# Performance work log

Measured on AMD Instinct MI355X. Metric: run time of the kernel, lower is better.

## Reference

```python
import jax, jax.numpy as jnp
import numpy as np

N_NODES = 100000
N_EDGES = 3200000
IN_DIM = 128
HIDDEN = 128
N_GRAPHS = 64


def setup_inputs() -> dict:
    key = jax.random.key(0)
    ks = jax.random.split(key, 16)
    feat = jax.random.normal(ks[0], (N_NODES, IN_DIM), dtype=jnp.float32)
    src = jax.random.randint(ks[1], (N_EDGES,), 0, N_NODES, dtype=jnp.int32)
    dst = jax.random.randint(ks[2], (N_EDGES,), 0, N_NODES, dtype=jnp.int32)
    graph_ids = jnp.sort(jax.random.randint(ks[3], (N_NODES,), 0, N_GRAPHS, dtype=jnp.int32))
    # GraphConv weights (in_feats, out_feats) + bias, DGL default glorot-ish scale
    def lin(k, fi, fo):
        s = 1.0 / np.sqrt(fi)
        kw, kb = jax.random.split(k)
        W = jax.random.uniform(kw, (fi, fo), jnp.float32, -s, s)
        b = jax.random.uniform(kb, (fo,), jnp.float32, -s, s)
        return W, b
    W1, b1 = lin(ks[4], IN_DIM, HIDDEN)
    W2, b2 = lin(ks[5], HIDDEN, HIDDEN)
    # MLPReadout(128, 1, L=3): 128->64->32->16->1
    Wm0, bm0 = lin(ks[6], 128, 64)
    Wm1, bm1 = lin(ks[7], 64, 32)
    Wm2, bm2 = lin(ks[8], 32, 16)
    Wm3, bm3 = lin(ks[9], 16, 1)
    return dict(feat=feat, src=src, dst=dst, graph_ids=graph_ids, num_graphs=N_GRAPHS,
                W1=W1, b1=b1, W2=W2, b2=b2,
                Wm0=Wm0, bm0=bm0, Wm1=Wm1, bm1=bm1, Wm2=Wm2, bm2=bm2, Wm3=Wm3, bm3=bm3)


def reference(feat, src, dst, graph_ids, num_graphs,
              W1, b1, W2, b2,
              Wm0, bm0, Wm1, bm1, Wm2, bm2, Wm3, bm3):
    N = feat.shape[0]
    ones_e = jnp.ones(src.shape[0], dtype=feat.dtype)
    # DGL GraphConv norm='both': D_out^{-1/2} on src side, D_in^{-1/2} on dst side,
    # degrees clamped to >=1 (allow_zero_in_degree=True)
    deg_out = jnp.clip(jax.ops.segment_sum(ones_e, src, num_segments=N), 1.0)
    deg_in = jnp.clip(jax.ops.segment_sum(ones_e, dst, num_segments=N), 1.0)
    norm_src = jax.lax.rsqrt(deg_out)[:, None]  # [N,1]
    norm_dst = jax.lax.rsqrt(deg_in)[:, None]

    def gconv(h, W, b):
        h = h * norm_src
        agg = jax.ops.segment_sum(h[src], dst, num_segments=N)  # SpMM: [N,d]
        return agg * norm_dst @ W + b

    h = jax.nn.relu(gconv(feat, W1, b1))
    h = jax.nn.relu(gconv(h, W2, b2))

    # dgl.mean_nodes: per-graph mean over nodes
    counts = jnp.clip(jax.ops.segment_sum(jnp.ones(N, dtype=h.dtype), graph_ids, num_segments=num_graphs), 1.0)
    hg = jax.ops.segment_sum(h, graph_ids, num_segments=num_graphs) / counts[:, None]  # [G, hidden]

    # MLPReadout
    y = jax.nn.relu(hg @ Wm0 + bm0)
    y = jax.nn.relu(y @ Wm1 + bm1)
    y = jax.nn.relu(y @ Wm2 + bm2)
    return y @ Wm3 + bm3  # [G, 1]
```

## Files before the change

### kernel.cpp

```cpp
#include <hip/hip_runtime.h>
#include <hip/hip_fp16.h>

#define N_NODES 100000
#define N_EDGES 3200000
#define DIM 128
#define NG 64
#define GS_CHUNKS 16

#define KSH 8
#define BKT 256
#define NBKT ((N_NODES + BKT - 1) / BKT)
#define CHUNK 8192
#define NBLK ((N_EDGES + CHUNK - 1) / CHUNK)

using f16x8 = __attribute__((ext_vector_type(8))) _Float16;
using f32x4 = __attribute__((ext_vector_type(4))) float;

__global__ __launch_bounds__(256) void k_hist1(const int* __restrict__ src, const int* __restrict__ dst,
                                               int* __restrict__ histD, int* __restrict__ histS,
                                               int* __restrict__ rowtot) {
    __shared__ int hD[4 * NBKT];
    __shared__ int hS[4 * NBKT];
    int t = threadIdx.x, blk = blockIdx.x;
    int w = t >> 6;
    for (int i = t; i < 4 * NBKT; i += 256) { hD[i] = 0; hS[i] = 0; }
    __syncthreads();
    int base = blk * CHUNK;
    for (int i = t; i < CHUNK; i += 256) {
        int e = base + i;
        if (e < N_EDGES) {
            atomicAdd(&hD[w * NBKT + (dst[e] >> KSH)], 1);
            atomicAdd(&hS[w * NBKT + (src[e] >> KSH)], 1);
        }
    }
    __syncthreads();
    for (int i = t; i < NBKT; i += 256) {
        int d = hD[i] + hD[NBKT + i] + hD[2 * NBKT + i] + hD[3 * NBKT + i];
        int s = hS[i] + hS[NBKT + i] + hS[2 * NBKT + i] + hS[3 * NBKT + i];
        histD[i * NBLK + blk] = d;
        histS[i * NBLK + blk] = s;
        atomicAdd(&rowtot[i], d);
        atomicAdd(&rowtot[NBKT + i], s);
    }
}

__global__ __launch_bounds__(512) void k_rowapply(int* __restrict__ histD, int* __restrict__ histS,
                                                  const int* __restrict__ rowtot) {
    __shared__ int sh[512];
    __shared__ int red[512];
    int r = blockIdx.x;
    int half = (r < NBKT) ? 0 : 1;
    int pos = half ? (r - NBKT) : r;
    int* a = half ? (histS + (size_t)pos * NBLK) : (histD + (size_t)pos * NBLK);
    int t = threadIdx.x;
    red[t] = (t < pos) ? rowtot[half * NBKT + t] : 0;
    __syncthreads();
    for (int off = 256; off > 0; off >>= 1) {
        if (t < off) red[t] += red[t + off];
        __syncthreads();
    }
    int basev = red[0];
    int x = (t < NBLK) ? a[t] : 0;
    sh[t] = x; __syncthreads();
    for (int off = 1; off < 512; off <<= 1) {
        int y = sh[t]; int u = (t >= off) ? sh[t - off] : 0;
        __syncthreads(); sh[t] = y + u; __syncthreads();
    }
    if (t < NBLK) a[t] = sh[t] - x + basev;
}

__global__ __launch_bounds__(256) void k_scatter1(const int* __restrict__ src, const int* __restrict__ dst,
                                                  const int* __restrict__ histD, const int* __restrict__ histS,
                                                  int* __restrict__ bufD, unsigned short* __restrict__ bufS) {
    __shared__ int gbD[NBKT], cntD[NBKT], offD[NBKT], curD[NBKT];
    __shared__ int gbS[NBKT], cntS[NBKT], offS[NBKT], curS[NBKT];
    __shared__ int stageD[CHUNK];
    __shared__ unsigned short stageS[CHUNK];
    int t = threadIdx.x, blk = blockIdx.x;
    for (int b = t; b < NBKT; b += 256) {
        int idx = b * NBLK + blk;
        int st = histD[idx];
        int nx = (idx + 1 < NBKT * NBLK) ? histD[idx + 1] : N_EDGES;
        gbD[b] = st; cntD[b] = nx - st;
        int st2 = histS[idx];
        int nx2 = (idx + 1 < NBKT * NBLK) ? histS[idx + 1] : N_EDGES;
        gbS[b] = st2; cntS[b] = nx2 - st2;
    }
    __syncthreads();
    if (t < 64) {
        int lane = t;
        int base7 = lane * 7;
        int loc[7]; int s7 = 0;
        #pragma unroll
        for (int k = 0; k < 7; k++) { int b = base7 + k; loc[k] = s7; s7 += (b < NBKT) ? cntD[b] : 0; }
        int x = s7;
        #pragma unroll
        for (int off = 1; off < 64; off <<= 1) { int y = __shfl_up(x, off); if (lane >= off) x += y; }
        int excl = x - s7;
        #pragma unroll
        for (int k = 0; k < 7; k++) { int b = base7 + k; if (b < NBKT) { offD[b] = excl + loc[k]; curD[b] = excl + loc[k]; } }
    } else if (t < 128) {
        int lane = t - 64;
        int base7 = lane * 7;
        int loc[7]; int s7 = 0;
        #pragma unroll
        for (int k = 0; k < 7; k++) { int b = base7 + k; loc[k] = s7; s7 += (b < NBKT) ? cntS[b] : 0; }
        int x = s7;
        #pragma unroll
        for (int off = 1; off < 64; off <<= 1) { int y = __shfl_up(x, off); if (lane >= off) x += y; }
        int excl = x - s7;
        #pragma unroll
        for (int k = 0; k < 7; k++) { int b = base7 + k; if (b < NBKT) { offS[b] = excl + loc[k]; curS[b] = excl + loc[k]; } }
    }
    __syncthreads();
    int base = blk * CHUNK;
    for (int i = t; i < CHUNK; i += 256) {
        int e = base + i;
        if (e < N_EDGES) {
            int s = src[e], d = dst[e];
            int pD = atomicAdd(&curD[d >> KSH], 1);
            stageD[pD] = ((d & (BKT - 1)) << 17) | s;
            int pS = atomicAdd(&curS[s >> KSH], 1);
            stageS[pS] = (unsigned short)(s & (BKT - 1));
        }
    }
    __syncthreads();
    int wv = t >> 6, lane = t & 63;
    for (int b = wv; b < NBKT; b += 4) {
        int c = cntD[b], o = offD[b], g = gbD[b];
        for (int i = lane; i < c; i += 64) bufD[g + i] = stageD[o + i];
        int c2 = cntS[b], o2 = offS[b], g2 = gbS[b];
        for (int i = lane; i < c2; i += 64) bufS[g2 + i] = stageS[o2 + i];
    }
}

__global__ __launch_bounds__(256) void k_pass2s(const unsigned short* __restrict__ bufS,
                                                const int* __restrict__ histS,
                                                float* __restrict__ norm_src) {
    __shared__ int binc[BKT];
    int b = blockIdx.x, t = threadIdx.x;
    int start = histS[b * NBLK];
    int end = (b + 1 < NBKT) ? histS[(b + 1) * NBLK] : N_EDGES;
    if (t < BKT) binc[t] = 0;
    __syncthreads();
    for (int i = start + t; i < end; i += 256) atomicAdd(&binc[bufS[i]], 1);
    __syncthreads();
    int nb = N_NODES - b * BKT; if (nb > BKT) nb = BKT;
    if (t < nb) {
        int c = binc[t]; if (c < 1) c = 1;
        norm_src[b * BKT + t] = rsqrtf((float)c);
    }
}

__global__ __launch_bounds__(256) void k_pass2(const int* __restrict__ bufD,
                                               const int* __restrict__ histD,
                                               int* __restrict__ rowptr, float* __restrict__ norm_dst,
                                               int* __restrict__ col) {
    __shared__ int binc[BKT];
    __shared__ int binoff[BKT];
    int b = blockIdx.x, t = threadIdx.x;
    int start = histD[b * NBLK];
    int end = (b + 1 < NBKT) ? histD[(b + 1) * NBLK] : N_EDGES;
    if (t < BKT) binc[t] = 0;
    __syncthreads();
    for (int i = start + t; i < end; i += 256) atomicAdd(&binc[bufD[i] >> 17], 1);
    __syncthreads();
    if (t < 64) {
        int base4 = t * 4;
        int loc[4]; int s4 = 0;
        #pragma unroll
        for (int k = 0; k < 4; k++) { loc[k] = s4; s4 += binc[base4 + k]; }
        int x = s4;
        #pragma unroll
        for (int off = 1; off < 64; off <<= 1) {
            int y = __shfl_up(x, off);
            if (t >= off) x += y;
        }
        int excl = x - s4;
        #pragma unroll
        for (int k = 0; k < 4; k++) binoff[base4 + k] = excl + loc[k];
    }
    __syncthreads();
    int nb = N_NODES - b * BKT; if (nb > BKT) nb = BKT;
    if (t < nb) {
        rowptr[b * BKT + t] = start + binoff[t];
        int c = binc[t]; if (c < 1) c = 1;
        norm_dst[b * BKT + t] = rsqrtf((float)c);
    }
    if (b == NBKT - 1 && t == 0) rowptr[N_NODES] = N_EDGES;
    __syncthreads();
    if (t < BKT) binc[t] = binoff[t];
    __syncthreads();
    for (int i = start + t; i < end; i += 256) {
        int v = bufD[i];
        int ld = v >> 17, s = v & 0x1FFFF;
        int p = atomicAdd(&binc[ld], 1);
        col[start + p] = s;
    }
}

__global__ __launch_bounds__(256) void k_cast8(const float* __restrict__ in,
                                               const float* __restrict__ norm_src,
                                               unsigned* __restrict__ out) {
    int i4 = blockIdx.x * 256 + threadIdx.x;
    const int TOT = N_NODES * DIM / 4;
    if (i4 >= TOT) return;
    int row = i4 >> 5;
    float sc = norm_src[row];
    float4 v = ((const float4*)in)[i4];
    unsigned w = 0;
    w = __builtin_amdgcn_cvt_pk_fp8_f32(v.x * sc, v.y * sc, w, 0);
    w = __builtin_amdgcn_cvt_pk_fp8_f32(v.z * sc, v.w * sc, w, 1);
    out[i4] = w;
}

#define ACC8(r) do {                                                                  \
    auto p0 = __builtin_amdgcn_cvt_pk_f32_fp8((r).x, 0); a0 += p0[0]; a1 += p0[1];    \
    auto p1 = __builtin_amdgcn_cvt_pk_f32_fp8((r).x, 1); a2 += p1[0]; a3 += p1[1];    \
    auto p2 = __builtin_amdgcn_cvt_pk_f32_fp8((r).y, 0); a4 += p2[0]; a5 += p2[1];    \
    auto p3 = __builtin_amdgcn_cvt_pk_f32_fp8((r).y, 1); a6 += p3[0]; a7 += p3[1];    \
    auto p4 = __builtin_amdgcn_cvt_pk_f32_fp8((r).z, 0); a8 += p4[0]; a9 += p4[1];    \
    auto p5 = __builtin_amdgcn_cvt_pk_f32_fp8((r).z, 1); a10 += p5[0]; a11 += p5[1];  \
    auto p6 = __builtin_amdgcn_cvt_pk_f32_fp8((r).w, 0); a12 += p6[0]; a13 += p6[1];  \
    auto p7 = __builtin_amdgcn_cvt_pk_f32_fp8((r).w, 1); a14 += p7[0]; a15 += p7[1];  \
} while (0)

__global__ __launch_bounds__(256) void k_spmm8(const unsigned char* __restrict__ in,
                       const int* __restrict__ rowptr, const int* __restrict__ col,
                       const float* __restrict__ norm_dst, __half2* __restrict__ out) {
    int wid = (blockIdx.x * 256 + threadIdx.x) >> 6;
    int lane = threadIdx.x & 63;
    int rg = lane >> 3, l8 = lane & 7;
    int node = wid * 8 + rg;
    if (node >= N_NODES) return;
    int jb = rowptr[node], je = rowptr[node + 1];
    float a0 = 0.f, a1 = 0.f, a2 = 0.f, a3 = 0.f, a4 = 0.f, a5 = 0.f, a6 = 0.f, a7 = 0.f;
    float a8 = 0.f, a9 = 0.f, a10 = 0.f, a11 = 0.f, a12 = 0.f, a13 = 0.f, a14 = 0.f, a15 = 0.f;
    int j = jb;
    for (; j + 2 <= je; j += 2) {
        int s0 = col[j], s1 = col[j + 1];
        uint4 r0 = *(const uint4*)&in[(size_t)s0 * 128 + l8 * 16];
        uint4 r1 = *(const uint4*)&in[(size_t)s1 * 128 + l8 * 16];
        ACC8(r0);
        ACC8(r1);
    }
    if (j < je) {
        int s0 = col[j];
        uint4 r0 = *(const uint4*)&in[(size_t)s0 * 128 + l8 * 16];
        ACC8(r0);
    }
    float nd = norm_dst[node];
    __half2 h0 = __floats2half2_rn(a0 * nd, a1 * nd);
    __half2 h1 = __floats2half2_rn(a2 * nd, a3 * nd);
    __half2 h2 = __floats2half2_rn(a4 * nd, a5 * nd);
    __half2 h3 = __floats2half2_rn(a6 * nd, a7 * nd);
    __half2 h4 = __floats2half2_rn(a8 * nd, a9 * nd);
    __half2 h5 = __floats2half2_rn(a10 * nd, a11 * nd);
    __half2 h6 = __floats2half2_rn(a12 * nd, a13 * nd);
    __half2 h7 = __floats2half2_rn(a14 * nd, a15 * nd);
    uint4 o0, o1;
    o0.x = *(unsigned*)&h0; o0.y = *(unsigned*)&h1;
    o0.z = *(unsigned*)&h2; o0.w = *(unsigned*)&h3;
    o1.x = *(unsigned*)&h4; o1.y = *(unsigned*)&h5;
    o1.z = *(unsigned*)&h6; o1.w = *(unsigned*)&h7;
    *(uint4*)&out[(size_t)node * 64 + l8 * 8] = o0;
    *(uint4*)&out[(size_t)node * 64 + l8 * 8 + 4] = o1;
}

template <bool SCALE, bool OUT8>
__global__ __launch_bounds__(256) void k_gemm_mfma(const __half* __restrict__ A,
        const float* __restrict__ W, const float* __restrict__ bias,
        const float* __restrict__ rowscale, void* __restrict__ outp) {
    __shared__ _Float16 lds[128 * 136];
    int tid = threadIdx.x;
    for (int idx = tid * 4; idx < DIM * DIM; idx += 256 * 4) {
        int k = idx >> 7, n = idx & 127;
        float4 w = *(const float4*)&W[idx];
        lds[(n + 0) * 136 + k] = (_Float16)w.x;
        lds[(n + 1) * 136 + k] = (_Float16)w.y;
        lds[(n + 2) * 136 + k] = (_Float16)w.z;
        lds[(n + 3) * 136 + k] = (_Float16)w.w;
    }
    __syncthreads();
    int wv = tid >> 6, lane = tid & 63;
    int rbase = blockIdx.x * 64 + wv * 16;
    int l15 = lane & 15, kg = lane >> 4;
    int arow = rbase + l15; if (arow >= N_NODES) arow = N_NODES - 1;
    const _Float16* Af = (const _Float16*)A + (size_t)arow * DIM + kg * 8;
    f16x8 a0 = *(const f16x8*)(Af + 0);
    f16x8 a1 = *(const f16x8*)(Af + 32);
    f16x8 a2 = *(const f16x8*)(Af + 64);
    f16x8 a3 = *(const f16x8*)(Af + 96);
    f32x4 acc[8];
    #pragma unroll
    for (int nt = 0; nt < 8; nt++) acc[nt] = (f32x4){0.f, 0.f, 0.f, 0.f};
    #pragma unroll
    for (int nt = 0; nt < 8; nt++) {
        const _Float16* bb = &lds[(nt * 16 + l15) * 136 + kg * 8];
        f16x8 b0 = *(const f16x8*)(bb + 0);
        f16x8 b1 = *(const f16x8*)(bb + 32);
        f16x8 b2 = *(const f16x8*)(bb + 64);
        f16x8 b3 = *(const f16x8*)(bb + 96);
        acc[nt] = __builtin_amdgcn_mfma_f32_16x16x32_f16(a0, b0, acc[nt], 0, 0, 0);
        acc[nt] = __builtin_amdgcn_mfma_f32_16x16x32_f16(a1, b1, acc[nt], 0, 0, 0);
        acc[nt] = __builtin_amdgcn_mfma_f32_16x16x32_f16(a2, b2, acc[nt], 0, 0, 0);
        acc[nt] = __builtin_amdgcn_mfma_f32_16x16x32_f16(a3, b3, acc[nt], 0, 0, 0);
    }
    __syncthreads();
    float bsc[4];
    #pragma unroll
    for (int r = 0; r < 4; r++) {
        if (SCALE) {
            int row = rbase + kg * 4 + r; if (row >= N_NODES) row = N_NODES - 1;
            bsc[r] = rowscale[row];
        } else bsc[r] = 1.f;
    }
    #pragma unroll
    for (int nt = 0; nt < 8; nt++) {
        float bv = bias[nt * 16 + l15];
        #pragma unroll
        for (int r = 0; r < 4; r++) {
            float v = fmaxf(acc[nt][r] + bv, 0.f) * bsc[r];
            lds[(size_t)(wv * 16 + kg * 4 + r) * 136 + nt * 16 + l15] = (_Float16)v;
        }
    }
    __syncthreads();
    #pragma unroll
    for (int t = 0; t < 4; t++) {
        int lrow = wv * 16 + t * 4 + kg;
        int grow = rbase + t * 4 + kg;
        f16x8 v = *(const f16x8*)&lds[(size_t)lrow * 136 + l15 * 8];
        if (grow < N_NODES) {
            if (OUT8) {
                unsigned w0 = 0, w1 = 0;
                w0 = __builtin_amdgcn_cvt_pk_fp8_f32((float)v[0], (float)v[1], w0, 0);
                w0 = __builtin_amdgcn_cvt_pk_fp8_f32((float)v[2], (float)v[3], w0, 1);
                w1 = __builtin_amdgcn_cvt_pk_fp8_f32((float)v[4], (float)v[5], w1, 0);
                w1 = __builtin_amdgcn_cvt_pk_fp8_f32((float)v[6], (float)v[7], w1, 1);
                uint2 o; o.x = w0; o.y = w1;
                *(uint2*)&((unsigned char*)outp)[(size_t)grow * 128 + l15 * 8] = o;
            } else {
                *(f16x8*)&((_Float16*)outp)[(size_t)grow * DIM + l15 * 8] = v;
            }
        }
    }
}

__global__ __launch_bounds__(256) void k_graphsum_part(const __half2* __restrict__ h,
                           const int* __restrict__ gids, float* __restrict__ partial) {
    __shared__ float redx[256];
    __shared__ float redy[256];
    __shared__ int sb[2];
    int g = blockIdx.x;
    int c = blockIdx.y;
    if (threadIdx.x == 0) {
        int lo = 0, hi = N_NODES;
        while (lo < hi) { int mid = (lo + hi) >> 1; if (gids[mid] < g) lo = mid + 1; else hi = mid; }
        sb[0] = lo;
        lo = 0; hi = N_NODES;
        while (lo < hi) { int mid = (lo + hi) >> 1; if (gids[mid] <= g) lo = mid + 1; else hi = mid; }
        sb[1] = lo;
    }
    __syncthreads();
    int s = sb[0], e = sb[1];
    int p = threadIdx.x & 63;
    int r = threadIdx.x >> 6;
    int clen = (e - s + GS_CHUNKS - 1) / GS_CHUNKS;
    int b0 = s + c * clen;
    int b1 = b0 + clen; if (b1 > e) b1 = e;
    float ax = 0.f, ay = 0.f;
    for (int nd = b0 + r; nd < b1; nd += 4) {
        float2 f = __half22float2(h[(size_t)nd * 64 + p]);
        ax += f.x; ay += f.y;
    }
    redx[threadIdx.x] = ax; redy[threadIdx.x] = ay;
    __syncthreads();
    if (threadIdx.x < 64) {
        float sx = redx[threadIdx.x] + redx[threadIdx.x + 64] + redx[threadIdx.x + 128] + redx[threadIdx.x + 192];
        float sy = redy[threadIdx.x] + redy[threadIdx.x + 64] + redy[threadIdx.x + 128] + redy[threadIdx.x + 192];
        float* pp = &partial[((size_t)g * GS_CHUNKS + c) * DIM];
        pp[2 * threadIdx.x] = sx;
        pp[2 * threadIdx.x + 1] = sy;
    }
}

__global__ __launch_bounds__(128) void k_mlp(const float* __restrict__ partial,
                      const int* __restrict__ gids,
                      const float* __restrict__ Wm0, const float* __restrict__ bm0,
                      const float* __restrict__ Wm1, const float* __restrict__ bm1,
                      const float* __restrict__ Wm2, const float* __restrict__ bm2,
                      const float* __restrict__ Wm3, const float* __restrict__ bm3,
                      float* __restrict__ out) {
    __shared__ float hb[DIM];
    __shared__ float l0[64];
    __shared__ float l1[32];
    __shared__ float l2[16];
    __shared__ int scnt;
    int g = blockIdx.x;
    int t = threadIdx.x;
    if (t == 0) {
        int lo = 0, hi = N_NODES;
        while (lo < hi) { int mid = (lo + hi) >> 1; if (gids[mid] < g) lo = mid + 1; else hi = mid; }
        int s = lo;
        lo = 0; hi = N_NODES;
        while (lo < hi) { int mid = (lo + hi) >> 1; if (gids[mid] <= g) lo = mid + 1; else hi = mid; }
        int c = lo - s; if (c < 1) c = 1;
        scnt = c;
    }
    __syncthreads();
    float acc = 0.f;
    #pragma unroll
    for (int c = 0; c < GS_CHUNKS; c++)
        acc += partial[((size_t)g * GS_CHUNKS + c) * DIM + t];
    hb[t] = acc / (float)scnt;
    __syncthreads();
    if (t < 64) {
        float a = bm0[t];
        for (int k = 0; k < 128; k++) a += hb[k] * Wm0[k * 64 + t];
        l0[t] = fmaxf(a, 0.f);
    }
    __syncthreads();
    if (t < 32) {
        float a = bm1[t];
        for (int k = 0; k < 64; k++) a += l0[k] * Wm1[k * 32 + t];
        l1[t] = fmaxf(a, 0.f);
    }
    __syncthreads();
    if (t < 16) {
        float a = bm2[t];
        for (int k = 0; k < 32; k++) a += l1[k] * Wm2[k * 16 + t];
        l2[t] = fmaxf(a, 0.f);
    }
    __syncthreads();
    if (t == 0) {
        float a = bm3[0];
        for (int k = 0; k < 16; k++) a += l2[k] * Wm3[k];
        out[g] = a;
    }
}

extern "C" void kernel_launch(void* const* d_in, const int* in_sizes, int n_in,
                              void* d_out, int out_size, void* d_ws, size_t ws_size,
                              hipStream_t stream) {
    const float* feat = (const float*)d_in[0];
    const int*   src  = (const int*)d_in[1];
    const int*   dst  = (const int*)d_in[2];
    const int*   gids = (const int*)d_in[3];
    const float* W1   = (const float*)d_in[5];
    const float* b1   = (const float*)d_in[6];
    const float* W2   = (const float*)d_in[7];
    const float* b2   = (const float*)d_in[8];
    const float* Wm0  = (const float*)d_in[9];
    const float* bm0  = (const float*)d_in[10];
    const float* Wm1  = (const float*)d_in[11];
    const float* bm1  = (const float*)d_in[12];
    const float* Wm2  = (const float*)d_in[13];
    const float* bm2  = (const float*)d_in[14];
    const float* Wm3  = (const float*)d_in[15];
    const float* bm3  = (const float*)d_in[16];
    float* out = (float*)d_out;

    char* ws = (char*)d_ws;
    size_t off = 0;
    auto alloc = [&](size_t bytes) -> void* {
        void* p = ws + off;
        off += (bytes + 511) & ~(size_t)511;
        return p;
    };
    float* norm_src = (float*)alloc((size_t)N_NODES * 4);
    float* norm_dst = (float*)alloc((size_t)N_NODES * 4);
    int* rowptr   = (int*)alloc((size_t)(N_NODES + 1) * 4);
    int* histD    = (int*)alloc((size_t)NBKT * NBLK * 4);
    int* histS    = (int*)alloc((size_t)NBKT * NBLK * 4);
    int* rowtot   = (int*)alloc((size_t)(2 * NBKT) * 4);
    int* bufD     = (int*)alloc((size_t)N_EDGES * 4);
    int* colbuf   = (int*)alloc((size_t)N_EDGES * 4);
    unsigned char* feat8 = (unsigned char*)alloc((size_t)N_NODES * DIM);
    unsigned char* h8    = (unsigned char*)alloc((size_t)N_NODES * DIM);
    __half* s16   = (__half*)alloc((size_t)N_NODES * DIM * 2);
    __half* g16   = (__half*)alloc((size_t)N_NODES * DIM * 2);
    float* partial = (float*)alloc((size_t)NG * GS_CHUNKS * DIM * 4);
    unsigned short* bufS = (unsigned short*)colbuf;
    int* col = colbuf;

    hipMemsetAsync(rowtot, 0, (size_t)(2 * NBKT) * 4, stream);

    k_hist1<<<NBLK, 256, 0, stream>>>(src, dst, histD, histS, rowtot);
    k_rowapply<<<2 * NBKT, 512, 0, stream>>>(histD, histS, rowtot);
    k_scatter1<<<NBLK, 256, 0, stream>>>(src, dst, histD, histS, bufD, bufS);
    k_pass2s<<<NBKT, 256, 0, stream>>>(bufS, histS, norm_src);
    k_pass2<<<NBKT, 256, 0, stream>>>(bufD, histD, rowptr, norm_dst, col);

    k_cast8<<<(N_NODES * DIM / 4 + 255) / 256, 256, 0, stream>>>(feat, norm_src, (unsigned*)feat8);

    int sb2 = (N_NODES + 31) / 32;
    int gb = (N_NODES + 63) / 64;
    k_spmm8<<<sb2, 256, 0, stream>>>(feat8, rowptr, col, norm_dst, (__half2*)s16);
    k_gemm_mfma<true, true><<<gb, 256, 0, stream>>>(s16, W1, b1, norm_src, h8);
    k_spmm8<<<sb2, 256, 0, stream>>>(h8, rowptr, col, norm_dst, (__half2*)s16);
    k_gemm_mfma<false, false><<<gb, 256, 0, stream>>>(s16, W2, b2, nullptr, g16);

    dim3 gsg(NG, GS_CHUNKS);
    k_graphsum_part<<<gsg, 256, 0, stream>>>((const __half2*)g16, gids, partial);
    k_mlp<<<NG, 128, 0, stream>>>(partial, gids, Wm0, bm0, Wm1, bm1, Wm2, bm2, Wm3, bm3, out);
}
```

Before: 351.6 us.

## Fuse src-degree, dst-CSR and feature fp8 cast into one kernel; unroll SpMM by four

Merges the source-degree pass, the destination CSR build pass and the fp8 feature cast into a single launch. The first half of the blocks build the CSR, and the second half compute norm_src and cast their bucket's feature rows using norm values held in shared memory. To let both halves run at once, bufS gets its own buffer instead of aliasing the col array. The SpMM inner loop is also unrolled to four edges per iteration to keep more gathers in flight, which costs extra registers.

```diff
diff --git a/kernel.cpp b/kernel.cpp
--- a/kernel.cpp
+++ b/kernel.cpp
@@ -134,84 +134,86 @@
     }
 }
 
-__global__ __launch_bounds__(256) void k_pass2s(const unsigned short* __restrict__ bufS,
-                                                const int* __restrict__ histS,
-                                                float* __restrict__ norm_src) {
-    __shared__ int binc[BKT];
-    int b = blockIdx.x, t = threadIdx.x;
-    int start = histS[b * NBLK];
-    int end = (b + 1 < NBKT) ? histS[(b + 1) * NBLK] : N_EDGES;
-    if (t < BKT) binc[t] = 0;
-    __syncthreads();
-    for (int i = start + t; i < end; i += 256) atomicAdd(&binc[bufS[i]], 1);
-    __syncthreads();
-    int nb = N_NODES - b * BKT; if (nb > BKT) nb = BKT;
-    if (t < nb) {
-        int c = binc[t]; if (c < 1) c = 1;
-        norm_src[b * BKT + t] = rsqrtf((float)c);
-    }
-}
-
-__global__ __launch_bounds__(256) void k_pass2(const int* __restrict__ bufD,
+__global__ __launch_bounds__(256) void k_pass2both(const int* __restrict__ bufD,
+                                               const unsigned short* __restrict__ bufS,
                                                const int* __restrict__ histD,
+                                               const int* __restrict__ histS,
+                                               const float* __restrict__ feat,
                                                int* __restrict__ rowptr, float* __restrict__ norm_dst,
-                                               int* __restrict__ col) {
+                                               float* __restrict__ norm_src,
+                                               int* __restrict__ col, unsigned* __restrict__ feat8) {
     __shared__ int binc[BKT];
     __shared__ int binoff[BKT];
-    int b = blockIdx.x, t = threadIdx.x;
-    int start = histD[b * NBLK];
-    int end = (b + 1 < NBKT) ? histD[(b + 1) * NBLK] : N_EDGES;
-    if (t < BKT) binc[t] = 0;
-    __syncthreads();
-    for (int i = start + t; i < end; i += 256) atomicAdd(&binc[bufD[i] >> 17], 1);
-    __syncthreads();
-    if (t < 64) {
-        int base4 = t * 4;
-        int loc[4]; int s4 = 0;
-        #pragma unroll
-        for (int k = 0; k < 4; k++) { loc[k] = s4; s4 += binc[base4 + k]; }
-        int x = s4;
-        #pragma unroll
-        for (int off = 1; off < 64; off <<= 1) {
-            int y = __shfl_up(x, off);
-            if (t >= off) x += y;
-        }
-        int excl = x - s4;
-        #pragma unroll
-        for (int k = 0; k < 4; k++) binoff[base4 + k] = excl + loc[k];
-    }
-    __syncthreads();
-    int nb = N_NODES - b * BKT; if (nb > BKT) nb = BKT;
-    if (t < nb) {
-        rowptr[b * BKT + t] = start + binoff[t];
-        int c = binc[t]; if (c < 1) c = 1;
-        norm_dst[b * BKT + t] = rsqrtf((float)c);
-    }
-    if (b == NBKT - 1 && t == 0) rowptr[N_NODES] = N_EDGES;
-    __syncthreads();
-    if (t < BKT) binc[t] = binoff[t];
-    __syncthreads();
-    for (int i = start + t; i < end; i += 256) {
-        int v = bufD[i];
-        int ld = v >> 17, s = v & 0x1FFFF;
-        int p = atomicAdd(&binc[ld], 1);
-        col[start + p] = s;
-    }
-}
-
-__global__ __launch_bounds__(256) void k_cast8(const float* __restrict__ in,
-                                               const float* __restrict__ norm_src,
-                                               unsigned* __restrict__ out) {
-    int i4 = blockIdx.x * 256 + threadIdx.x;
-    const int TOT = N_NODES * DIM / 4;
-    if (i4 >= TOT) return;
-    int row = i4 >> 5;
-    float sc = norm_src[row];
-    float4 v = ((const float4*)in)[i4];
-    unsigned w = 0;
-    w = __builtin_amdgcn_cvt_pk_fp8_f32(v.x * sc, v.y * sc, w, 0);
-    w = __builtin_amdgcn_cvt_pk_fp8_f32(v.z * sc, v.w * sc, w, 1);
-    out[i4] = w;
+    __shared__ float snorm[BKT];
+    int bb = blockIdx.x, t = threadIdx.x;
+    if (bb < NBKT) {
+        int b = bb;
+        int start = histD[b * NBLK];
+        int end = (b + 1 < NBKT) ? histD[(b + 1) * NBLK] : N_EDGES;
+        if (t < BKT) binc[t] = 0;
+        __syncthreads();
+        for (int i = start + t; i < end; i += 256) atomicAdd(&binc[bufD[i] >> 17], 1);
+        __syncthreads();
+        if (t < 64) {
+            int base4 = t * 4;
+            int loc[4]; int s4 = 0;
+            #pragma unroll
+            for (int k = 0; k < 4; k++) { loc[k] = s4; s4 += binc[base4 + k]; }
+            int x = s4;
+            #pragma unroll
+            for (int off = 1; off < 64; off <<= 1) {
+                int y = __shfl_up(x, off);
+                if (t >= off) x += y;
+            }
+            int excl = x - s4;
+            #pragma unroll
+            for (int k = 0; k < 4; k++) binoff[base4 + k] = excl + loc[k];
+        }
+        __syncthreads();
+        int nb = N_NODES - b * BKT; if (nb > BKT) nb = BKT;
+        if (t < nb) {
+            rowptr[b * BKT + t] = start + binoff[t];
+            int c = binc[t]; if (c < 1) c = 1;
+            norm_dst[b * BKT + t] = rsqrtf((float)c);
+        }
+        if (b == NBKT - 1 && t == 0) rowptr[N_NODES] = N_EDGES;
+        __syncthreads();
+        if (t < BKT) binc[t] = binoff[t];
+        __syncthreads();
+        for (int i = start + t; i < end; i += 256) {
+            int v = bufD[i];
+            int ld = v >> 17, s = v & 0x1FFFF;
+            int p = atomicAdd(&binc[ld], 1);
+            col[start + p] = s;
+        }
+    } else {
+        int b = bb - NBKT;
+        int start = histS[b * NBLK];
+        int end = (b + 1 < NBKT) ? histS[(b + 1) * NBLK] : N_EDGES;
+        if (t < BKT) binc[t] = 0;
+        __syncthreads();
+        for (int i = start + t; i < end; i += 256) atomicAdd(&binc[bufS[i]], 1);
+        __syncthreads();
+        int nb = N_NODES - b * BKT; if (nb > BKT) nb = BKT;
+        if (t < nb) {
+            int c = binc[t]; if (c < 1) c = 1;
+            float sc = rsqrtf((float)c);
+            norm_src[b * BKT + t] = sc;
+            snorm[t] = sc;
+        }
+        __syncthreads();
+        const float4* fin = (const float4*)feat;
+        int nq = nb * 32;
+        for (int i = t; i < nq; i += 256) {
+            int nl = i >> 5, q = i & 31;
+            float sc = snorm[nl];
+            float4 v = fin[((size_t)(b * BKT + nl)) * 32 + q];
+            unsigned w = 0;
+            w = __builtin_amdgcn_cvt_pk_fp8_f32(v.x * sc, v.y * sc, w, 0);
+            w = __builtin_amdgcn_cvt_pk_fp8_f32(v.z * sc, v.w * sc, w, 1);
+            feat8[((size_t)(b * BKT + nl)) * 32 + q] = w;
+        }
+    }
 }
 
 #define ACC8(r) do {                                                                  \
@@ -237,12 +239,24 @@
     float a0 = 0.f, a1 = 0.f, a2 = 0.f, a3 = 0.f, a4 = 0.f, a5 = 0.f, a6 = 0.f, a7 = 0.f;
     float a8 = 0.f, a9 = 0.f, a10 = 0.f, a11 = 0.f, a12 = 0.f, a13 = 0.f, a14 = 0.f, a15 = 0.f;
     int j = jb;
-    for (; j + 2 <= je; j += 2) {
+    for (; j + 4 <= je; j += 4) {
+        int s0 = col[j], s1 = col[j + 1], s2 = col[j + 2], s3 = col[j + 3];
+        uint4 r0 = *(const uint4*)&in[(size_t)s0 * 128 + l8 * 16];
+        uint4 r1 = *(const uint4*)&in[(size_t)s1 * 128 + l8 * 16];
+        uint4 r2 = *(const uint4*)&in[(size_t)s2 * 128 + l8 * 16];
+        uint4 r3 = *(const uint4*)&in[(size_t)s3 * 128 + l8 * 16];
+        ACC8(r0);
+        ACC8(r1);
+        ACC8(r2);
+        ACC8(r3);
+    }
+    if (j + 2 <= je) {
         int s0 = col[j], s1 = col[j + 1];
         uint4 r0 = *(const uint4*)&in[(size_t)s0 * 128 + l8 * 16];
         uint4 r1 = *(const uint4*)&in[(size_t)s1 * 128 + l8 * 16];
         ACC8(r0);
         ACC8(r1);
+        j += 2;
     }
     if (j < je) {
         int s0 = col[j];
@@ -474,24 +488,21 @@
     int* histS    = (int*)alloc((size_t)NBKT * NBLK * 4);
     int* rowtot   = (int*)alloc((size_t)(2 * NBKT) * 4);
     int* bufD     = (int*)alloc((size_t)N_EDGES * 4);
-    int* colbuf   = (int*)alloc((size_t)N_EDGES * 4);
+    unsigned short* bufS = (unsigned short*)alloc((size_t)N_EDGES * 2);
+    int* col      = (int*)alloc((size_t)N_EDGES * 4);
     unsigned char* feat8 = (unsigned char*)alloc((size_t)N_NODES * DIM);
     unsigned char* h8    = (unsigned char*)alloc((size_t)N_NODES * DIM);
     __half* s16   = (__half*)alloc((size_t)N_NODES * DIM * 2);
     __half* g16   = (__half*)alloc((size_t)N_NODES * DIM * 2);
     float* partial = (float*)alloc((size_t)NG * GS_CHUNKS * DIM * 4);
-    unsigned short* bufS = (unsigned short*)colbuf;
-    int* col = colbuf;
 
     hipMemsetAsync(rowtot, 0, (size_t)(2 * NBKT) * 4, stream);
 
     k_hist1<<<NBLK, 256, 0, stream>>>(src, dst, histD, histS, rowtot);
     k_rowapply<<<2 * NBKT, 512, 0, stream>>>(histD, histS, rowtot);
     k_scatter1<<<NBLK, 256, 0, stream>>>(src, dst, histD, histS, bufD, bufS);
-    k_pass2s<<<NBKT, 256, 0, stream>>>(bufS, histS, norm_src);
-    k_pass2<<<NBKT, 256, 0, stream>>>(bufD, histD, rowptr, norm_dst, col);
-
-    k_cast8<<<(N_NODES * DIM / 4 + 255) / 256, 256, 0, stream>>>(feat, norm_src, (unsigned*)feat8);
+    k_pass2both<<<2 * NBKT, 256, 0, stream>>>(bufD, bufS, histD, histS, feat,
+                                              rowptr, norm_dst, norm_src, col, (unsigned*)feat8);
 
     int sb2 = (N_NODES + 31) / 32;
     int gb = (N_NODES + 63) / 64;
```

Result: faster. 332.8 us (-5.3%).
